# Kernel optimization log

Measured on AMD Instinct MI355X. Metric: run time of the kernel, lower is better.

Reference implementation:

```python
import jax, jax.numpy as jnp
import numpy as np
import math

D_MODEL = 64
N_HEAD = 8
BATCH = 16
NTOK = 511  # pads to 512 in original torch code; padn = 1 > 0


def setup_inputs() -> dict:
    key = jax.random.key(0)
    ks = jax.random.split(key, 4)
    scl = 0.005
    x = jax.random.normal(ks[0], (BATCH, NTOK, D_MODEL), jnp.float32)
    wq_w = scl * jax.random.normal(ks[1], (N_HEAD * D_MODEL, D_MODEL + 1), jnp.float32)
    wq_w = wq_w.at[:, -1].set(0.0)  # bias column zeroed at init
    wv_w = scl * jax.random.normal(ks[2], (N_HEAD * D_MODEL, D_MODEL + 1), jnp.float32)
    wv_w = wv_w.at[:, -1].set(0.0)
    wk = scl * jnp.ones((N_HEAD, D_MODEL), jnp.float32)
    fanout_w = scl * jax.random.normal(ks[3], (D_MODEL, D_MODEL + 1), jnp.float32)
    fanout_w = fanout_w.at[:, -1].set(0.0)
    return {"x": x, "wq_w": wq_w, "wv_w": wv_w, "wk": wk, "fanout_w": fanout_w}


def _linear_m(w, x):
    # LinearM: w[:, :-1] is weight, w[:, -1] is bias
    return jnp.einsum('oi,bti->bto', w[:, :-1], x) + w[:, -1]


def _l1_logits(q, k):
    # q, k: [b, t, h, w]. Returns [b, s(key), d(query), h] =
    #   -(1/sqrt(w)) * sum_w |q[b,d,h,w] - k[b,s,h,w]|
    # Scan over the width axis so we never materialize a [b,t,t,h,w] tensor.
    b, t, h, w = q.shape
    scale = 1.0 / math.sqrt(w)
    qw = jnp.moveaxis(q, -1, 0)  # [w, b, t, h]
    kw = jnp.moveaxis(k, -1, 0)

    def body(acc, qk):
        qi, ki = qk  # each [b, t, h]
        return acc + jnp.abs(qi[:, None, :, :] - ki[:, :, None, :]), None

    acc0 = jnp.zeros((b, t, t, h), q.dtype)
    acc, _ = jax.lax.scan(body, acc0, (qw, kw))
    return -acc * scale


def reference(x, wq_w, wv_w, wk, fanout_w):
    b, t, dm = x.shape
    q = _linear_m(wq_w, x).reshape(b, t, N_HEAD, D_MODEL)
    v = _linear_m(wv_w, x).reshape(b, t, N_HEAD, D_MODEL)
    # k: x broadcast over heads, elementwise-gated by wk
    k = x[:, :, None, :] * wk[None, None, :, :]  # [b, t, h, w]
    logits = _l1_logits(q, k)  # [b, s, d, h]
    # Extra zero-logit 'sink' key row (the original zero-padded row with a[:,t,:,:]=0)
    sink = jnp.zeros((b, 1, t, N_HEAD), logits.dtype)
    logits = jnp.concatenate([logits, sink], axis=1)  # [b, t+1, d, h]
    a = jax.nn.softmax(logits, axis=1)[:, :t]  # softmax over keys+sink, drop sink
    # einsum 'bsdh,bshw->bdhw' then sum over h, fused:
    out = jnp.einsum('bsdh,bshw->bdw', a, v)  # [b, t, d_model]
    y = jax.nn.relu(out)  # module's self.gelu is actually nn.ReLU()
    y = _linear_m(fanout_w, y)
    return x + y
```

## Files before the change

### kernel.cpp

```cpp
#include <hip/hip_runtime.h>
#include <stdint.h>


#define B  16
#define H  8
#define T  511
#define ANUMSZ ((size_t)B * T * H * 64)
#define DENSZ  ((size_t)B * T * H)

typedef __fp16 f16x2 __attribute__((ext_vector_type(2)));
typedef __fp16 f16x8 __attribute__((ext_vector_type(8)));
typedef float  f32x4 __attribute__((ext_vector_type(4)));
typedef __attribute__((address_space(3))) uint32_t lds_u32;
typedef __attribute__((address_space(1))) const uint32_t glb_u32;

#if __has_builtin(__builtin_amdgcn_exp2f)
#define EXP2F(x) __builtin_amdgcn_exp2f(x)
#else
#define EXP2F(x) exp2f(x)
#endif

__device__ __forceinline__ uint32_t SAD(uint32_t a, uint32_t b, uint32_t c) {
#if __has_builtin(__builtin_amdgcn_sad_u8)
  return __builtin_amdgcn_sad_u8(a, b, c);
#else
  uint32_t d;
  asm("v_sad_u8 %0, %1, %2, %3" : "=v"(d) : "v"(a), "v"(b), "v"(c));
  return d;
#endif
}

__device__ __forceinline__ uint32_t PKRTZ(float a, float b) {
  f16x2 r = __builtin_amdgcn_cvt_pkrtz(a, b);
  return __builtin_bit_cast(uint32_t, r);
}

__device__ __forceinline__ uint32_t quantu8(float v) {
  float q = __builtin_rintf(__builtin_fmaf(v, 256.f, 128.f));
  q = fminf(fmaxf(q, 0.f), 255.f);
  return (uint32_t)(int)q;
}

__global__ void wtrans_kernel(const float* __restrict__ wq, const float* __restrict__ wv,
                              const float* __restrict__ wf, float* __restrict__ wt,
                              float* __restrict__ bias, float* __restrict__ wft,
                              float* __restrict__ biasf) {
  const int idx = blockIdx.x * 256 + (int)threadIdx.x;
  if (idx < 64 * 1024) {
    const int k = idx >> 10, j = idx & 1023;
    const float* src = (j < 512) ? wq : wv;
    const int oc = j & 511;
    wt[idx] = src[oc * 65 + k];
    if (k == 0) bias[j] = src[oc * 65 + 64];
  } else if (idx < 64 * 1024 + 64 * 64) {
    const int r = idx - 64 * 1024;
    const int k = r >> 6, w = r & 63;
    wft[r] = wf[w * 65 + k];
    if (k == 0) biasf[w] = wf[w * 65 + 64];
  }
}

__global__ void __launch_bounds__(256, 2) proj_kernel(
    const float* __restrict__ x, const float* __restrict__ wt,
    const float* __restrict__ bias, const float* __restrict__ wk,
    uint8_t* __restrict__ qq, _Float16* __restrict__ vt,
    uint8_t* __restrict__ kq) {
  __shared__ float xt[64][16];
  const int b = blockIdx.y, tc = blockIdx.x;
  const int t0 = tc * 16;
  const int tid = threadIdx.x;
  {
    const int tl = tid >> 4, k0 = (tid & 15) * 4;
    const int t = t0 + tl;
    float4 v = {0.f, 0.f, 0.f, 0.f};
    if (t < T) v = *(const float4*)(x + ((size_t)b * T + t) * 64 + k0);
    xt[k0 + 0][tl] = v.x; xt[k0 + 1][tl] = v.y;
    xt[k0 + 2][tl] = v.z; xt[k0 + 3][tl] = v.w;
  }
  __syncthreads();
  const int j0 = tid * 4;
  const float4 bs = *(const float4*)(bias + j0);
  float4 acc[16];
#pragma unroll
  for (int t = 0; t < 16; ++t) acc[t] = bs;
#pragma unroll 4
  for (int k = 0; k < 64; ++k) {
    const float4 w4 = *(const float4*)(wt + (size_t)k * 1024 + j0);
    const float4* xr = (const float4*)xt[k];
    const float4 xa = xr[0], xb = xr[1], xc = xr[2], xd = xr[3];
    const float xv[16] = {xa.x, xa.y, xa.z, xa.w, xb.x, xb.y, xb.z, xb.w,
                          xc.x, xc.y, xc.z, xc.w, xd.x, xd.y, xd.z, xd.w};
#pragma unroll
    for (int t = 0; t < 16; ++t) {
      acc[t].x = __builtin_fmaf(w4.x, xv[t], acc[t].x);
      acc[t].y = __builtin_fmaf(w4.y, xv[t], acc[t].y);
      acc[t].z = __builtin_fmaf(w4.z, xv[t], acc[t].z);
      acc[t].w = __builtin_fmaf(w4.w, xv[t], acc[t].w);
    }
  }
  const int oc = j0 & 511;
  const int hh = oc >> 6, w0 = oc & 63;
  const size_t bh = (size_t)b * H + hh;
  if (j0 < 512) {
#pragma unroll
    for (int t = 0; t < 16; ++t) {
      if (t0 + t < T) {
        const uint32_t u = quantu8(acc[t].x) | (quantu8(acc[t].y) << 8) |
                           (quantu8(acc[t].z) << 16) | (quantu8(acc[t].w) << 24);
        *(uint32_t*)(qq + (bh * T + (size_t)(t0 + t)) * 64 + w0) = u;
      }
    }
  } else {
#pragma unroll
    for (int i = 0; i < 4; ++i) {
      uint32_t u[8];
      const float* a = (const float*)acc;
#pragma unroll
      for (int m = 0; m < 8; ++m) u[m] = PKRTZ(a[4 * (2 * m) + i], a[4 * (2 * m + 1) + i]);
      _Float16* p = vt + (bh * 64 + (size_t)(w0 + i)) * 512 + t0;
      *(uint4*)(p)     = make_uint4(u[0], u[1], u[2], u[3]);
      *(uint4*)(p + 8) = make_uint4(u[4], u[5], u[6], u[7]);
    }
  }
  const int tk = tid >> 4, w4 = (tid & 15) * 4;
  if (t0 + tk < T) {
    const float xv0 = xt[w4 + 0][tk], xv1 = xt[w4 + 1][tk];
    const float xv2 = xt[w4 + 2][tk], xv3 = xt[w4 + 3][tk];
#pragma unroll
    for (int hh2 = 0; hh2 < H; ++hh2) {
      const float4 wkv = *(const float4*)(wk + hh2 * 64 + w4);
      const uint32_t u = quantu8(xv0 * wkv.x) | (quantu8(xv1 * wkv.y) << 8) |
                         (quantu8(xv2 * wkv.z) << 16) | (quantu8(xv3 * wkv.w) << 24);
      *(uint32_t*)(kq + (((size_t)b * H + hh2) * T + (size_t)(t0 + tk)) * 64 + w4) = u;
    }
  }
}

__global__ void __launch_bounds__(256, 4) attn_kernel(
    const uint8_t* __restrict__ qq, const uint8_t* __restrict__ kq,
    const _Float16* __restrict__ vt, _Float16* __restrict__ anumP,
    float* __restrict__ denp) {
  __shared__ uint4 klds[512];
  const int bx = blockIdx.x, h = blockIdx.y, b = blockIdx.z;
  const int qt = bx & 3, kh = bx >> 2;
  const int bh = b * H + h;
  const int tid = threadIdx.x;
  const int kbeg = kh * 128;
  {
    const uint8_t* kgb = kq + ((size_t)bh * T + kbeg) * 64;
#pragma unroll
    for (int it = 0; it < 2; ++it) {
      const int d = it * 256 + tid;
      const int s = d >> 2, j = d & 3;
      const int sj = j ^ ((s >> 3) & 3);
      const uint8_t* gsrc = kgb + (size_t)(s * 4 + sj) * 16;
      uint32_t* ldst = (uint32_t*)(klds + it * 256 + (tid >> 6) * 64);
      __builtin_amdgcn_global_load_lds((glb_u32*)gsrc, (lds_u32*)ldst, 16, 0, 0);
    }
  }
  const int wave = tid >> 6, lane = tid & 63;
  const int c = lane & 15, g = lane >> 4;
  const int qb = qt * 128 + wave * 32;
  uint4 q[2][4];
#pragma unroll
  for (int m = 0; m < 2; ++m) {
    const int qm = qb + 16 * m + c;
    const int qsafe = qm < T ? qm : T - 1;
    const uint4* qp = (const uint4*)(qq + ((size_t)bh * T + qsafe) * 64);
#pragma unroll
    for (int i = 0; i < 4; ++i) q[m][i] = qp[i];
  }
  const _Float16* vb = vt + (size_t)bh * 64 * 512;
  f32x4 acc[2][4];
#pragma unroll
  for (int m = 0; m < 2; ++m)
#pragma unroll
    for (int nt = 0; nt < 4; ++nt) acc[m][nt] = f32x4{0.f, 0.f, 0.f, 0.f};
  float den[2] = {0.f, 0.f};
  const float Cl = -0x1.715476p+0f / 2048.0f;
  __syncthreads();

#pragma unroll 1
  for (int kt = 0; kt < 4; ++kt) {
    const int s0 = kbeg + kt * 32;
    const _Float16* vp0 = vb + (size_t)c * 512 + s0 + g * 8;
    uint4 bvec[4];
#pragma unroll
    for (int nt = 0; nt < 4; ++nt) bvec[nt] = *(const uint4*)(vp0 + nt * 16 * 512);
    uint32_t pk[2][4];
#pragma unroll
    for (int jj = 0; jj < 4; ++jj) {
      float pp[2][2];
#pragma unroll
      for (int e = 0; e < 2; ++e) {
        const int s = s0 + g * 8 + jj * 2 + e;
        const int sl = (s < T ? s : T - 1) - kbeg;
        const uint4* kp = klds + sl * 4;
        const int bb = (sl >> 3) & 3;
        const uint4 k0 = kp[bb], k1 = kp[1 ^ bb], k2 = kp[2 ^ bb], k3 = kp[3 ^ bb];
        const bool live = s < T;
#pragma unroll
        for (int m = 0; m < 2; ++m) {
          uint32_t a0 = 0, a1 = 0;
          a0 = SAD(q[m][0].x, k0.x, a0); a0 = SAD(q[m][0].y, k0.y, a0);
          a0 = SAD(q[m][0].z, k0.z, a0); a0 = SAD(q[m][0].w, k0.w, a0);
          a0 = SAD(q[m][1].x, k1.x, a0); a0 = SAD(q[m][1].y, k1.y, a0);
          a0 = SAD(q[m][1].z, k1.z, a0); a0 = SAD(q[m][1].w, k1.w, a0);
          a1 = SAD(q[m][2].x, k2.x, a1); a1 = SAD(q[m][2].y, k2.y, a1);
          a1 = SAD(q[m][2].z, k2.z, a1); a1 = SAD(q[m][2].w, k2.w, a1);
          a1 = SAD(q[m][3].x, k3.x, a1); a1 = SAD(q[m][3].y, k3.y, a1);
          a1 = SAD(q[m][3].z, k3.z, a1); a1 = SAD(q[m][3].w, k3.w, a1);
          const float p = EXP2F((float)(a0 + a1) * Cl);
          pp[m][e] = live ? p : 0.f;
        }
      }
#pragma unroll
      for (int m = 0; m < 2; ++m) {
        den[m] += pp[m][0] + pp[m][1];
        pk[m][jj] = PKRTZ(pp[m][0], pp[m][1]);
      }
    }
#pragma unroll
    for (int m = 0; m < 2; ++m) {
      const f16x8 af = __builtin_bit_cast(f16x8, make_uint4(pk[m][0], pk[m][1], pk[m][2], pk[m][3]));
#pragma unroll
      for (int nt = 0; nt < 4; ++nt) {
        const f16x8 bf = __builtin_bit_cast(f16x8, bvec[nt]);
        acc[m][nt] = __builtin_amdgcn_mfma_f32_16x16x32_f16(af, bf, acc[m][nt], 0, 0, 0);
      }
    }
  }

#pragma unroll
  for (int m = 0; m < 2; ++m) {
    den[m] += __shfl_xor(den[m], 16, 64);
    den[m] += __shfl_xor(den[m], 32, 64);
  }
  if (g == 0) {
#pragma unroll
    for (int m = 0; m < 2; ++m) {
      const int qd = qb + 16 * m + c;
      if (qd < T) denp[(size_t)kh * DENSZ + ((size_t)b * T + qd) * H + h] = den[m];
    }
  }
  _Float16* abase = anumP + (size_t)kh * ANUMSZ;
#pragma unroll
  for (int m = 0; m < 2; ++m) {
#pragma unroll
    for (int r = 0; r < 4; ++r) {
      const int qr = qb + 16 * m + g * 4 + r;
      if (qr < T) {
        _Float16* ap = abase + (((size_t)b * T + qr) * H + h) * 64 + c;
        ap[0]  = (_Float16)acc[m][0][r];
        ap[16] = (_Float16)acc[m][1][r];
        ap[32] = (_Float16)acc[m][2][r];
        ap[48] = (_Float16)acc[m][3][r];
      }
    }
  }
}

__global__ void __launch_bounds__(256) finalize_kernel(
    const float* __restrict__ x, const _Float16* __restrict__ anumP,
    const float* __restrict__ denp, const float* __restrict__ wft,
    const float* __restrict__ biasf, float* __restrict__ out) {
  __shared__ float u[4][64];
  __shared__ float rd[4][8];
  const int tid = threadIdx.x;
  const int lt = tid >> 6, w = tid & 63;
  const int gt = blockIdx.x * 4 + lt;
  if (w < 8) {
    float d = 1.0f;
#pragma unroll
    for (int kh = 0; kh < 4; ++kh) d += denp[(size_t)kh * DENSZ + (size_t)gt * H + w];
    rd[lt][w] = 1.0f / d;
  }
  __syncthreads();
  float s = 0.f;
#pragma unroll
  for (int hh = 0; hh < H; ++hh) {
    float n = 0.f;
#pragma unroll
    for (int kh = 0; kh < 4; ++kh)
      n += (float)anumP[(size_t)kh * ANUMSZ + ((size_t)gt * H + hh) * 64 + w];
    s += n * rd[lt][hh];
  }
  u[lt][w] = fmaxf(s, 0.f);
  __syncthreads();
  float y = biasf[w];
#pragma unroll 8
  for (int k = 0; k < 64; ++k) y = __builtin_fmaf(wft[k * 64 + w], u[lt][k], y);
  out[(size_t)gt * 64 + w] = x[(size_t)gt * 64 + w] + y;
}

extern "C" void kernel_launch(void* const* d_in, const int* in_sizes, int n_in,
                              void* d_out, int out_size, void* d_ws, size_t ws_size,
                              hipStream_t stream) {
  (void)in_sizes; (void)n_in; (void)out_size; (void)ws_size;
  const float* x  = (const float*)d_in[0];
  const float* wq = (const float*)d_in[1];
  const float* wv = (const float*)d_in[2];
  const float* wk = (const float*)d_in[3];
  const float* wf = (const float*)d_in[4];
  float* out = (float*)d_out;

  uint8_t* ws = (uint8_t*)d_ws;
  const size_t o_qq   = 0;
  const size_t o_kq   = 4186112;
  const size_t o_vt   = 8372224;
  const size_t o_anum = 16760832;
  const size_t o_den  = 50249728;
  const size_t o_wt   = 51296256;
  const size_t o_bias = 51558400;
  const size_t o_wft  = 51562496;
  const size_t o_bf   = 51578880;

  uint8_t*  qq    = ws + o_qq;
  uint8_t*  kq    = ws + o_kq;
  _Float16* vt    = (_Float16*)(ws + o_vt);
  _Float16* anum  = (_Float16*)(ws + o_anum);
  float*    denp  = (float*)(ws + o_den);
  float*    wt    = (float*)(ws + o_wt);
  float*    bias  = (float*)(ws + o_bias);
  float*    wft   = (float*)(ws + o_wft);
  float*    biasf = (float*)(ws + o_bf);

  wtrans_kernel<<<dim3((64 * 1024 + 64 * 64 + 255) / 256), 256, 0, stream>>>(
      wq, wv, wf, wt, bias, wft, biasf);
  proj_kernel<<<dim3(32, B), 256, 0, stream>>>(x, wt, bias, wk, qq, vt, kq);
  attn_kernel<<<dim3(16, H, B), 256, 0, stream>>>(qq, kq, vt, anum, denp);
  finalize_kernel<<<dim3(B * T / 4), 256, 0, stream>>>(x, anum, denp, wft, biasf, out);
}
```

Baseline: 83.12 us.

## Compute quantized K inside attention kernel and shrink projection token tile

The quantized K buffer is no longer written by the projection kernel. Each attention block instead reads x and wk directly, quantizes K rows on the fly and stores them to LDS with the same swizzle. This drops the kq global round trip and the async global-to-LDS copy. The projection kernel's token tile also halves from 16 to 8 with twice as many blocks and higher occupancy bounds, at the cost of re-reading the weights more often and recomputing K in each of the four query-tile blocks.

```diff
diff --git a/kernel.cpp b/kernel.cpp
--- a/kernel.cpp
+++ b/kernel.cpp
@@ -11,8 +11,6 @@
 typedef __fp16 f16x2 __attribute__((ext_vector_type(2)));
 typedef __fp16 f16x8 __attribute__((ext_vector_type(8)));
 typedef float  f32x4 __attribute__((ext_vector_type(4)));
-typedef __attribute__((address_space(3))) uint32_t lds_u32;
-typedef __attribute__((address_space(1))) const uint32_t glb_u32;
 
 #if __has_builtin(__builtin_amdgcn_exp2f)
 #define EXP2F(x) __builtin_amdgcn_exp2f(x)
@@ -60,38 +58,36 @@
   }
 }
 
-__global__ void __launch_bounds__(256, 2) proj_kernel(
+__global__ void __launch_bounds__(256, 4) proj_kernel(
     const float* __restrict__ x, const float* __restrict__ wt,
-    const float* __restrict__ bias, const float* __restrict__ wk,
-    uint8_t* __restrict__ qq, _Float16* __restrict__ vt,
-    uint8_t* __restrict__ kq) {
-  __shared__ float xt[64][16];
+    const float* __restrict__ bias, uint8_t* __restrict__ qq,
+    _Float16* __restrict__ vt) {
+  __shared__ float xt[64][8];
   const int b = blockIdx.y, tc = blockIdx.x;
-  const int t0 = tc * 16;
+  const int t0 = tc * 8;
   const int tid = threadIdx.x;
-  {
-    const int tl = tid >> 4, k0 = (tid & 15) * 4;
-    const int t = t0 + tl;
-    float4 v = {0.f, 0.f, 0.f, 0.f};
-    if (t < T) v = *(const float4*)(x + ((size_t)b * T + t) * 64 + k0);
-    xt[k0 + 0][tl] = v.x; xt[k0 + 1][tl] = v.y;
-    xt[k0 + 2][tl] = v.z; xt[k0 + 3][tl] = v.w;
+  if (tid < 128) {
+    const int tok = tid >> 4, k0 = (tid & 15) * 4;
+    const int t = t0 + tok;
+    float4 val = {0.f, 0.f, 0.f, 0.f};
+    if (t < T) val = *(const float4*)(x + ((size_t)b * T + t) * 64 + k0);
+    xt[k0 + 0][tok] = val.x; xt[k0 + 1][tok] = val.y;
+    xt[k0 + 2][tok] = val.z; xt[k0 + 3][tok] = val.w;
   }
   __syncthreads();
   const int j0 = tid * 4;
   const float4 bs = *(const float4*)(bias + j0);
-  float4 acc[16];
-#pragma unroll
-  for (int t = 0; t < 16; ++t) acc[t] = bs;
-#pragma unroll 4
+  float4 acc[8];
+#pragma unroll
+  for (int t = 0; t < 8; ++t) acc[t] = bs;
+#pragma unroll 8
   for (int k = 0; k < 64; ++k) {
     const float4 w4 = *(const float4*)(wt + (size_t)k * 1024 + j0);
     const float4* xr = (const float4*)xt[k];
-    const float4 xa = xr[0], xb = xr[1], xc = xr[2], xd = xr[3];
-    const float xv[16] = {xa.x, xa.y, xa.z, xa.w, xb.x, xb.y, xb.z, xb.w,
-                          xc.x, xc.y, xc.z, xc.w, xd.x, xd.y, xd.z, xd.w};
-#pragma unroll
-    for (int t = 0; t < 16; ++t) {
+    const float4 xa = xr[0], xb = xr[1];
+    const float xv[8] = {xa.x, xa.y, xa.z, xa.w, xb.x, xb.y, xb.z, xb.w};
+#pragma unroll
+    for (int t = 0; t < 8; ++t) {
       acc[t].x = __builtin_fmaf(w4.x, xv[t], acc[t].x);
       acc[t].y = __builtin_fmaf(w4.y, xv[t], acc[t].y);
       acc[t].z = __builtin_fmaf(w4.z, xv[t], acc[t].z);
@@ -103,7 +99,7 @@
   const size_t bh = (size_t)b * H + hh;
   if (j0 < 512) {
 #pragma unroll
-    for (int t = 0; t < 16; ++t) {
+    for (int t = 0; t < 8; ++t) {
       if (t0 + t < T) {
         const uint32_t u = quantu8(acc[t].x) | (quantu8(acc[t].y) << 8) |
                            (quantu8(acc[t].z) << 16) | (quantu8(acc[t].w) << 24);
@@ -113,33 +109,20 @@
   } else {
 #pragma unroll
     for (int i = 0; i < 4; ++i) {
-      uint32_t u[8];
+      uint32_t u[4];
       const float* a = (const float*)acc;
 #pragma unroll
-      for (int m = 0; m < 8; ++m) u[m] = PKRTZ(a[4 * (2 * m) + i], a[4 * (2 * m + 1) + i]);
+      for (int m = 0; m < 4; ++m) u[m] = PKRTZ(a[4 * (2 * m) + i], a[4 * (2 * m + 1) + i]);
       _Float16* p = vt + (bh * 64 + (size_t)(w0 + i)) * 512 + t0;
-      *(uint4*)(p)     = make_uint4(u[0], u[1], u[2], u[3]);
-      *(uint4*)(p + 8) = make_uint4(u[4], u[5], u[6], u[7]);
-    }
-  }
-  const int tk = tid >> 4, w4 = (tid & 15) * 4;
-  if (t0 + tk < T) {
-    const float xv0 = xt[w4 + 0][tk], xv1 = xt[w4 + 1][tk];
-    const float xv2 = xt[w4 + 2][tk], xv3 = xt[w4 + 3][tk];
-#pragma unroll
-    for (int hh2 = 0; hh2 < H; ++hh2) {
-      const float4 wkv = *(const float4*)(wk + hh2 * 64 + w4);
-      const uint32_t u = quantu8(xv0 * wkv.x) | (quantu8(xv1 * wkv.y) << 8) |
-                         (quantu8(xv2 * wkv.z) << 16) | (quantu8(xv3 * wkv.w) << 24);
-      *(uint32_t*)(kq + (((size_t)b * H + hh2) * T + (size_t)(t0 + tk)) * 64 + w4) = u;
+      *(uint4*)(p) = make_uint4(u[0], u[1], u[2], u[3]);
     }
   }
 }
 
 __global__ void __launch_bounds__(256, 4) attn_kernel(
-    const uint8_t* __restrict__ qq, const uint8_t* __restrict__ kq,
-    const _Float16* __restrict__ vt, _Float16* __restrict__ anumP,
-    float* __restrict__ denp) {
+    const float* __restrict__ x, const float* __restrict__ wk,
+    const uint8_t* __restrict__ qq, const _Float16* __restrict__ vt,
+    _Float16* __restrict__ anumP, float* __restrict__ denp) {
   __shared__ uint4 klds[512];
   const int bx = blockIdx.x, h = blockIdx.y, b = blockIdx.z;
   const int qt = bx & 3, kh = bx >> 2;
@@ -147,15 +130,26 @@
   const int tid = threadIdx.x;
   const int kbeg = kh * 128;
   {
-    const uint8_t* kgb = kq + ((size_t)bh * T + kbeg) * 64;
+    const float* xb = x + (size_t)b * T * 64;
+    const float* wkh = wk + h * 64;
 #pragma unroll
     for (int it = 0; it < 2; ++it) {
       const int d = it * 256 + tid;
-      const int s = d >> 2, j = d & 3;
-      const int sj = j ^ ((s >> 3) & 3);
-      const uint8_t* gsrc = kgb + (size_t)(s * 4 + sj) * 16;
-      uint32_t* ldst = (uint32_t*)(klds + it * 256 + (tid >> 6) * 64);
-      __builtin_amdgcn_global_load_lds((glb_u32*)gsrc, (lds_u32*)ldst, 16, 0, 0);
+      const int s = d >> 2, jd = d & 3;
+      const int jl = jd ^ ((s >> 3) & 3);
+      const int row = kbeg + s;
+      const int rsafe = row < T ? row : T - 1;
+      const float* xr = xb + (size_t)rsafe * 64 + jl * 16;
+      const float* wr = wkh + jl * 16;
+      uint32_t u[4];
+#pragma unroll
+      for (int m = 0; m < 4; ++m) {
+        const float4 xv = *(const float4*)(xr + m * 4);
+        const float4 wv = *(const float4*)(wr + m * 4);
+        u[m] = quantu8(xv.x * wv.x) | (quantu8(xv.y * wv.y) << 8) |
+               (quantu8(xv.z * wv.z) << 16) | (quantu8(xv.w * wv.w) << 24);
+      }
+      klds[d] = make_uint4(u[0], u[1], u[2], u[3]);
     }
   }
   const int wave = tid >> 6, lane = tid & 63;
@@ -306,17 +300,15 @@
 
   uint8_t* ws = (uint8_t*)d_ws;
   const size_t o_qq   = 0;
-  const size_t o_kq   = 4186112;
-  const size_t o_vt   = 8372224;
-  const size_t o_anum = 16760832;
-  const size_t o_den  = 50249728;
-  const size_t o_wt   = 51296256;
-  const size_t o_bias = 51558400;
-  const size_t o_wft  = 51562496;
-  const size_t o_bf   = 51578880;
+  const size_t o_vt   = 4186112;
+  const size_t o_anum = 12574720;
+  const size_t o_den  = 46063616;
+  const size_t o_wt   = 47110144;
+  const size_t o_bias = 47372288;
+  const size_t o_wft  = 47376384;
+  const size_t o_bf   = 47392768;
 
   uint8_t*  qq    = ws + o_qq;
-  uint8_t*  kq    = ws + o_kq;
   _Float16* vt    = (_Float16*)(ws + o_vt);
   _Float16* anum  = (_Float16*)(ws + o_anum);
   float*    denp  = (float*)(ws + o_den);
@@ -327,7 +319,7 @@
 
   wtrans_kernel<<<dim3((64 * 1024 + 64 * 64 + 255) / 256), 256, 0, stream>>>(
       wq, wv, wf, wt, bias, wft, biasf);
-  proj_kernel<<<dim3(32, B), 256, 0, stream>>>(x, wt, bias, wk, qq, vt, kq);
-  attn_kernel<<<dim3(16, H, B), 256, 0, stream>>>(qq, kq, vt, anum, denp);
+  proj_kernel<<<dim3(64, B), 256, 0, stream>>>(x, wt, bias, qq, vt);
+  attn_kernel<<<dim3(16, H, B), 256, 0, stream>>>(x, wk, qq, vt, anum, denp);
   finalize_kernel<<<dim3(B * T / 4), 256, 0, stream>>>(x, anum, denp, wft, biasf, out);
 }
```

Result: slower. 85.67 us (+3.1%).
